# Optimization experiments

Measured on AMD Instinct MI355X. Metric: run time of the kernel, lower is better.

Reference implementation:

```python
import jax, jax.numpy as jnp
import numpy as np

S = 3072      # total tokens across all images
DIM = 1280    # hidden_size
H = 16        # num_heads
HD = DIM // H # head_dim = 80
NSEG = 6      # number of images (cu_seqlens has NSEG+1 entries)


def _rotate_half(x):
    x1, x2 = jnp.split(x, 2, axis=-1)
    return jnp.concatenate([-x2, x1], axis=-1)


def setup_inputs() -> dict:
    key = jax.random.key(0)
    ks = jax.random.split(key, 12)
    hidden_states = jax.random.normal(ks[0], (S, DIM), jnp.float32)
    # realistic vision rotary embedding: half-dim inv_freq, repeated to head_dim
    inv_freq = 1.0 / (10000.0 ** (jnp.arange(0, HD // 2, dtype=jnp.float32) / (HD // 2)))
    freqs = jnp.arange(S, dtype=jnp.float32)[:, None] * inv_freq[None, :]  # [S, HD/2]
    emb = jnp.concatenate([freqs, freqs], axis=-1)  # [S, HD]
    cos = jnp.cos(emb)
    sin = jnp.sin(emb)
    sc = 0.02
    wq = jax.random.normal(ks[1], (DIM, DIM), jnp.float32) * sc
    bq = jax.random.normal(ks[2], (DIM,), jnp.float32) * sc
    wk = jax.random.normal(ks[3], (DIM, DIM), jnp.float32) * sc
    bk = jax.random.normal(ks[4], (DIM,), jnp.float32) * sc
    wv = jax.random.normal(ks[5], (DIM, DIM), jnp.float32) * sc
    bv = jax.random.normal(ks[6], (DIM,), jnp.float32) * sc
    wo = jax.random.normal(ks[7], (DIM, DIM), jnp.float32) * sc
    bo = jax.random.normal(ks[8], (DIM,), jnp.float32) * sc
    cu_seqlens = (jnp.arange(NSEG + 1, dtype=jnp.int32) * (S // NSEG))  # [0,512,...,3072]
    return dict(hidden_states=hidden_states, cos=cos, sin=sin,
                wq=wq, bq=bq, wk=wk, bk=bk, wv=wv, bv=bv, wo=wo, bo=bo,
                cu_seqlens=cu_seqlens)


def reference(hidden_states, cos, sin, wq, bq, wk, bk, wv, bv, wo, bo, cu_seqlens):
    seq_length = hidden_states.shape[0]
    scaling = HD ** (-0.5)
    # QKV projections (torch Linear: x @ W.T + b)
    q = (hidden_states @ wq.T + bq).reshape(seq_length, H, HD)
    k = (hidden_states @ wk.T + bk).reshape(seq_length, H, HD)
    v = (hidden_states @ wv.T + bv).reshape(seq_length, H, HD)
    # apply_rotary_pos_emb_vision: cos/sin [S, HD] broadcast over head axis
    c = cos[:, None, :]
    s = sin[:, None, :]
    q = q * c + _rotate_half(q) * s
    k = k * c + _rotate_half(k) * s
    # block-diagonal (per-image) attention via segment mask
    seg = jnp.searchsorted(cu_seqlens[1:], jnp.arange(seq_length), side='right')
    mask = seg[:, None] == seg[None, :]  # [S, S] bool
    scores = jnp.einsum('shd,thd->hst', q, k) * scaling  # [H, S, S]
    scores = jnp.where(mask[None, :, :], scores, jnp.finfo(scores.dtype).min)
    attn = jax.nn.softmax(scores, axis=-1)
    out = jnp.einsum('hst,thd->shd', attn, v).reshape(seq_length, DIM)
    return out @ wo.T + bo
```

## Files before the change

### kernel.cpp

```cpp
#include <hip/hip_runtime.h>
#include <hip/hip_bf16.h>
#include <hip/hip_fp16.h>
#include <cstdint>
#include <cstddef>

typedef _Float16 f16;
typedef f16 f16x2 __attribute__((ext_vector_type(2)));
typedef f16 f16x4 __attribute__((ext_vector_type(4)));
typedef f16 f16x8 __attribute__((ext_vector_type(8)));
typedef float f32x4 __attribute__((ext_vector_type(4)));

#define S_LEN 3072
#define DIM 1280
#define NH 16
#define HD 80
#define SEG 512

#define MFMA16F(a, b, c) __builtin_amdgcn_mfma_f32_16x16x32_f16((a), (b), (c), 0, 0, 0)

__device__ __forceinline__ void gl2lds16(const void* g, void* l) {
    __builtin_amdgcn_global_load_lds(
        (const __attribute__((address_space(1))) unsigned int*)g,
        (__attribute__((address_space(3))) unsigned int*)l, 16, 0, 0);
}

__device__ __forceinline__ unsigned int pack2(float a, float b) {
    f16x2 t = {(f16)a, (f16)b};
    union { f16x2 v; unsigned int u; } c;
    c.v = t;
    return c.u;
}

__global__ __launch_bounds__(256) void cvt_kernel(
    const float* __restrict__ hs,
    const float* __restrict__ wq, const float* __restrict__ wk,
    const float* __restrict__ wv, const float* __restrict__ wo,
    f16* __restrict__ hs16,
    f16* __restrict__ wq16, f16* __restrict__ wk16,
    f16* __restrict__ wv16, f16* __restrict__ wo16)
{
    const int m = blockIdx.y;
    const float* src; f16* dst; int n4;
    if (m == 0)      { src = hs; dst = hs16; n4 = S_LEN * DIM / 4; }
    else if (m == 1) { src = wq; dst = wq16; n4 = DIM * DIM / 4; }
    else if (m == 2) { src = wk; dst = wk16; n4 = DIM * DIM / 4; }
    else if (m == 3) { src = wv; dst = wv16; n4 = DIM * DIM / 4; }
    else             { src = wo; dst = wo16; n4 = DIM * DIM / 4; }
    int idx = blockIdx.x * 256 + threadIdx.x;
    if (idx >= n4) return;
    f32x4 v = *(const f32x4*)(src + (size_t)idx * 4);
    f16x4 o;
#pragma unroll
    for (int e = 0; e < 4; ++e) o[e] = (f16)v[e];
    *(f16x4*)(dst + (size_t)idx * 4) = o;
}

__global__ __launch_bounds__(512, 2) void gemm_qkv192(
    const f16* __restrict__ A, const f16* __restrict__ Wb,
    const float* __restrict__ bq, const float* __restrict__ bk,
    const float* __restrict__ bv,
    f16* __restrict__ q16, f16* __restrict__ k16, f16* __restrict__ vT)
{
    const int bid = blockIdx.x;
    const int xcd = bid & 7;
    const int idx = bid >> 3;
    const int mt = xcd * 2 + idx / 15;
    const int nt = idx % 15;
    const int m0 = mt * 192;
    const int n0 = nt * 256;

    __shared__ __align__(16) f16 Abuf[2][192 * 64];
    __shared__ __align__(16) f16 Bbuf[2][256 * 64];

    const int tid = threadIdx.x;
    const int w = tid >> 6;
    const int lane = tid & 63;
    const int lane15 = lane & 15;
    const int quad = lane >> 4;
    const int wm = (w >> 2) * 96;
    const int wn = (w & 3) * 64;

    const int srow = lane >> 3;
    const int schk = (lane & 7) ^ srow;

    const int aRow = w * 24;
    const int bRow = (w & 3) * 64 + (w >> 2) * 16;

    const f16* gA = A + (size_t)(m0 + aRow + srow) * DIM + schk * 8;
    const f16* gB = Wb + (size_t)(n0 + bRow + srow) * DIM + schk * 8;

    const int x7 = lane15 & 7;
    const int cc0 = (quad ^ x7) * 8;
    const int cc1 = ((quad + 4) ^ x7) * 8;

    f32x4 acc[6][4];
#pragma unroll
    for (int i = 0; i < 6; ++i)
#pragma unroll
        for (int j = 0; j < 4; ++j)
            acc[i][j] = (f32x4){0.f, 0.f, 0.f, 0.f};

    {
        f16* lA = Abuf[0] + aRow * 64;
        gl2lds16(gA, lA);
        gl2lds16(gA + 8 * DIM, lA + 512);
        gl2lds16(gA + 16 * DIM, lA + 1024);
        f16* lB = Bbuf[0] + bRow * 64;
        gl2lds16(gB, lB);
        gl2lds16(gB + 8 * DIM, lB + 512);
        gl2lds16(gB + 32 * DIM, lB + 2048);
        gl2lds16(gB + 40 * DIM, lB + 2560);
    }

    for (int kt = 0; kt < 20; ++kt) {
        const int s = kt & 1;
        const int sn = s ^ 1;
        const int kn = (kt < 19) ? (kt + 1) : 19;
        const f16* As = Abuf[s];
        const f16* Bsl = Bbuf[s];
        const f16* gAn = gA + kn * 64;
        const f16* gBn = gB + kn * 64;

        asm volatile("s_waitcnt vmcnt(2)" ::: "memory");
        __builtin_amdgcn_s_barrier();
        __builtin_amdgcn_sched_barrier(0);
        {
            f16* lA = Abuf[sn] + aRow * 64;
            gl2lds16(gAn, lA);
            gl2lds16(gAn + 8 * DIM, lA + 512);
            gl2lds16(gAn + 16 * DIM, lA + 1024);
        }
        f16x8 a0[3][2], b01[2][2];
#pragma unroll
        for (int i = 0; i < 3; ++i) {
            const f16* rp = As + (wm + i * 16 + lane15) * 64;
            a0[i][0] = *(const f16x8*)(rp + cc0);
            a0[i][1] = *(const f16x8*)(rp + cc1);
        }
#pragma unroll
        for (int j = 0; j < 2; ++j) {
            const f16* rp = Bsl + (wn + j * 16 + lane15) * 64;
            b01[j][0] = *(const f16x8*)(rp + cc0);
            b01[j][1] = *(const f16x8*)(rp + cc1);
        }
        __builtin_amdgcn_s_setprio(1);
#pragma unroll
        for (int i = 0; i < 3; ++i)
#pragma unroll
            for (int j = 0; j < 2; ++j) {
                acc[i][j] = MFMA16F(a0[i][0], b01[j][0], acc[i][j]);
                acc[i][j] = MFMA16F(a0[i][1], b01[j][1], acc[i][j]);
            }
        __builtin_amdgcn_s_setprio(0);

        asm volatile("s_waitcnt vmcnt(3)" ::: "memory");
        __builtin_amdgcn_s_barrier();
        __builtin_amdgcn_sched_barrier(0);
        {
            f16* lB = Bbuf[sn] + bRow * 64;
            gl2lds16(gBn, lB);
            gl2lds16(gBn + 8 * DIM, lB + 512);
        }
        f16x8 b23[2][2];
#pragma unroll
        for (int j = 0; j < 2; ++j) {
            const f16* rp = Bsl + (wn + 32 + j * 16 + lane15) * 64;
            b23[j][0] = *(const f16x8*)(rp + cc0);
            b23[j][1] = *(const f16x8*)(rp + cc1);
        }
        __builtin_amdgcn_s_setprio(1);
#pragma unroll
        for (int i = 0; i < 3; ++i)
#pragma unroll
            for (int j = 0; j < 2; ++j) {
                acc[i][j + 2] = MFMA16F(a0[i][0], b23[j][0], acc[i][j + 2]);
                acc[i][j + 2] = MFMA16F(a0[i][1], b23[j][1], acc[i][j + 2]);
            }
        __builtin_amdgcn_s_setprio(0);

        __builtin_amdgcn_s_barrier();
        __builtin_amdgcn_sched_barrier(0);
        {
            f16* lB = Bbuf[sn] + bRow * 64 + 2048;
            gl2lds16(gBn + 32 * DIM, lB);
            gl2lds16(gBn + 40 * DIM, lB + 512);
        }
        f16x8 a1[3][2];
#pragma unroll
        for (int i = 0; i < 3; ++i) {
            const f16* rp = As + (wm + 48 + i * 16 + lane15) * 64;
            a1[i][0] = *(const f16x8*)(rp + cc0);
            a1[i][1] = *(const f16x8*)(rp + cc1);
        }
        __builtin_amdgcn_s_setprio(1);
#pragma unroll
        for (int i = 0; i < 3; ++i)
#pragma unroll
            for (int j = 0; j < 2; ++j) {
                acc[i + 3][j + 2] = MFMA16F(a1[i][0], b23[j][0], acc[i + 3][j + 2]);
                acc[i + 3][j + 2] = MFMA16F(a1[i][1], b23[j][1], acc[i + 3][j + 2]);
            }
        __builtin_amdgcn_s_setprio(0);

        __builtin_amdgcn_s_barrier();
        __builtin_amdgcn_sched_barrier(0);
        __builtin_amdgcn_s_setprio(1);
#pragma unroll
        for (int i = 0; i < 3; ++i)
#pragma unroll
            for (int j = 0; j < 2; ++j) {
                acc[i + 3][j] = MFMA16F(a1[i][0], b01[j][0], acc[i + 3][j]);
                acc[i + 3][j] = MFMA16F(a1[i][1], b01[j][1], acc[i + 3][j]);
            }
        __builtin_amdgcn_s_setprio(0);
    }
    asm volatile("s_waitcnt vmcnt(0)" ::: "memory");

    const int sel = nt / 5;
    const int nc0 = (nt % 5) * 256 + wn;
    const float* bias = (sel == 0) ? bq : (sel == 1) ? bk : bv;
    float bvv[4];
#pragma unroll
    for (int j = 0; j < 4; ++j) bvv[j] = bias[nc0 + j * 16 + lane15];

    if (sel < 2) {
        f16* O = sel ? k16 : q16;
#pragma unroll
        for (int i = 0; i < 6; ++i)
#pragma unroll
            for (int j = 0; j < 4; ++j)
#pragma unroll
                for (int r = 0; r < 4; ++r) {
                    int row = m0 + wm + i * 16 + quad * 4 + r;
                    O[(size_t)row * DIM + nc0 + j * 16 + lane15] =
                        (f16)(acc[i][j][r] + bvv[j]);
                }
    } else {
#pragma unroll
        for (int i = 0; i < 6; ++i)
#pragma unroll
            for (int j = 0; j < 4; ++j) {
                f16x4 ov;
#pragma unroll
                for (int r = 0; r < 4; ++r) ov[r] = (f16)(acc[i][j][r] + bvv[j]);
                int row = m0 + wm + i * 16 + quad * 4;
                int col = nc0 + j * 16 + lane15;
                *(f16x4*)(vT + (size_t)col * S_LEN + row) = ov;
            }
    }
}

__global__ __launch_bounds__(256) void gemm_out_kernel(
    const f16* __restrict__ A, const f16* __restrict__ W,
    const float* __restrict__ bias, float* __restrict__ OF)
{
    const int f = blockIdx.x;
    const int xcd = f & 7;
    const int idx = f >> 3;
    const int xt = xcd * 6 + idx % 6;
    const int yt = idx / 6;

    __shared__ __align__(16) f16 As[64 * 32];
    __shared__ __align__(16) f16 Bs[128 * 32];

    const int tid = threadIdx.x;
    const int lane = tid & 63;
    const int lane15 = tid & 15;
    const int quad = lane >> 4;
    const int w = tid >> 6;
    const int wn = w * 32;
    const int m0 = xt * 64;
    const int n0 = yt * 128;

    const int srA = w * 16 + (lane >> 2);
    const int srB = w * 32 + (lane >> 2);
    const int scol = (lane & 3) * 8;
    const f16* gA0 = A + (size_t)(m0 + srA) * DIM + scol;
    const f16* gB0 = W + (size_t)(n0 + srB) * DIM + scol;
    const f16* gB1 = W + (size_t)(n0 + srB + 16) * DIM + scol;
    f16* lA0 = As + (w * 16) * 32;
    f16* lB0 = Bs + (w * 32) * 32;
    f16* lB1 = Bs + (w * 32 + 16) * 32;

    f32x4 acc[4][2];
#pragma unroll
    for (int i = 0; i < 4; ++i)
#pragma unroll
        for (int j = 0; j < 2; ++j)
            acc[i][j] = (f32x4){0.f, 0.f, 0.f, 0.f};

    for (int kt = 0; kt < DIM / 32; ++kt) {
        __syncthreads();
        gl2lds16(gA0 + kt * 32, lA0);
        gl2lds16(gB0 + kt * 32, lB0);
        gl2lds16(gB1 + kt * 32, lB1);
        __syncthreads();

        f16x8 fa[4], fb[2];
#pragma unroll
        for (int i = 0; i < 4; ++i)
            fa[i] = *(const f16x8*)(As + (i * 16 + lane15) * 32 + quad * 8);
#pragma unroll
        for (int j = 0; j < 2; ++j)
            fb[j] = *(const f16x8*)(Bs + (wn + j * 16 + lane15) * 32 + quad * 8);
#pragma unroll
        for (int i = 0; i < 4; ++i)
#pragma unroll
            for (int j = 0; j < 2; ++j)
                acc[i][j] = MFMA16F(fa[i], fb[j], acc[i][j]);
    }

    float bvv[2];
#pragma unroll
    for (int j = 0; j < 2; ++j)
        bvv[j] = bias[n0 + wn + j * 16 + lane15];

#pragma unroll
    for (int i = 0; i < 4; ++i)
#pragma unroll
        for (int j = 0; j < 2; ++j)
#pragma unroll
            for (int r = 0; r < 4; ++r) {
                int row = m0 + i * 16 + quad * 4 + r;
                int col = n0 + wn + j * 16 + lane15;
                OF[(size_t)row * DIM + col] = acc[i][j][r] + bvv[j];
            }
}

__global__ __launch_bounds__(256) void rope_kernel(
    f16* __restrict__ qb, f16* __restrict__ kb,
    const float* __restrict__ cosb, const float* __restrict__ sinb)
{
    int idx = blockIdx.x * 256 + threadIdx.x;
    int c = idx % 5;
    int t = idx / 5;
    int h = t & 15; t >>= 4;
    int s = t % S_LEN;
    int which = t / S_LEN;
    f16* buf = which ? kb : qb;
    float scale = which ? 1.0f : 0.11180339887498948f;
    int j = c * 8;
    f32x4 ca = *(const f32x4*)(cosb + s * HD + j);
    f32x4 cb = *(const f32x4*)(cosb + s * HD + j + 4);
    f32x4 sna = *(const f32x4*)(sinb + s * HD + j);
    f32x4 snb = *(const f32x4*)(sinb + s * HD + j + 4);
    size_t base = (size_t)s * DIM + h * HD + j;
    f16x8 x1 = *(f16x8*)(buf + base);
    f16x8 x2 = *(f16x8*)(buf + base + 40);
    f16x8 o1, o2;
#pragma unroll
    for (int e = 0; e < 8; ++e) {
        float ce = (e < 4) ? ca[e] : cb[e - 4];
        float se = (e < 4) ? sna[e] : snb[e - 4];
        float a = (float)x1[e], b = (float)x2[e];
        o1[e] = (f16)((a * ce - b * se) * scale);
        o2[e] = (f16)((b * ce + a * se) * scale);
    }
    *(f16x8*)(buf + base) = o1;
    *(f16x8*)(buf + base + 40) = o2;
}

__global__ __launch_bounds__(256) void attn_kernel(
    const f16* __restrict__ q, const f16* __restrict__ k,
    const f16* __restrict__ vT, f16* __restrict__ o)
{
    const int h = blockIdx.x;
    const int g = blockIdx.y;
    const int qc = blockIdx.z;
    const int tid = threadIdx.x;
    const int lane15 = tid & 15;
    const int quad = (tid & 63) >> 4;
    const int w = tid >> 6;
    const int qbase = g * SEG + qc * 64;
    const int qrow = qbase + w * 16 + lane15;

    __shared__ __align__(16) f16 Ks[128 * 88];
    __shared__ __align__(16) f16 Vt[80 * 128];

    f16x8 zf;
#pragma unroll
    for (int e = 0; e < 8; ++e) zf[e] = (f16)0.0f;

    f16x8 fq[3];
#pragma unroll
    for (int kc = 0; kc < 3; ++kc) {
        if (kc == 2 && quad >= 2) fq[kc] = zf;
        else fq[kc] = *(const f16x8*)(q + (size_t)qrow * DIM + h * HD + kc * 32 + quad * 8);
    }

    float m_run = -1e30f, l_run = 0.f;
    f32x4 Oa[5];
#pragma unroll
    for (int dt = 0; dt < 5; ++dt) Oa[dt] = (f32x4){0.f, 0.f, 0.f, 0.f};

    for (int kt = 0; kt < 4; ++kt) {
        __syncthreads();
        const int kb = g * SEG + kt * 128;
#pragma unroll
        for (int c = tid; c < 1280; c += 256) {
            int r = c / 10;
            int c8 = (c - r * 10) * 8;
            *(f16x8*)(Ks + r * 88 + c8) =
                *(const f16x8*)(k + (size_t)(kb + r) * DIM + h * HD + c8);
        }
#pragma unroll
        for (int c = tid; c < 1280; c += 256) {
            int d = c >> 4;
            int sc = c & 15;
            *(f16x8*)(Vt + d * 128 + (sc ^ (d & 7)) * 8) =
                *(const f16x8*)(vT + (size_t)(h * HD + d) * S_LEN + kb + sc * 8);
        }
        __syncthreads();

        f32x4 sa[8];
#pragma unroll
        for (int nt = 0; nt < 8; ++nt) sa[nt] = (f32x4){0.f, 0.f, 0.f, 0.f};
#pragma unroll
        for (int kc = 0; kc < 3; ++kc) {
#pragma unroll
            for (int nt = 0; nt < 8; ++nt) {
                f16x8 fk;
                if (kc == 2 && quad >= 2) fk = zf;
                else fk = *(const f16x8*)(Ks + (nt * 16 + lane15) * 88 + kc * 32 + quad * 8);
                sa[nt] = MFMA16F(fk, fq[kc], sa[nt]);
            }
        }

        float mt = -1e30f;
#pragma unroll
        for (int nt = 0; nt < 8; ++nt)
#pragma unroll
            for (int r = 0; r < 4; ++r) mt = fmaxf(mt, sa[nt][r]);
        mt = fmaxf(mt, __shfl_xor(mt, 16, 64));
        mt = fmaxf(mt, __shfl_xor(mt, 32, 64));

        float mn = fmaxf(m_run, mt);
        float alpha = __expf(m_run - mn);
        m_run = mn;
        float lt = 0.f;
        unsigned int pp[8][2];
#pragma unroll
        for (int nt = 0; nt < 8; ++nt) {
            float p0 = __expf(sa[nt][0] - mn);
            float p1 = __expf(sa[nt][1] - mn);
            float p2 = __expf(sa[nt][2] - mn);
            float p3 = __expf(sa[nt][3] - mn);
            lt += (p0 + p1) + (p2 + p3);
            pp[nt][0] = pack2(p0, p1);
            pp[nt][1] = pack2(p2, p3);
        }
        lt += __shfl_xor(lt, 16, 64);
        lt += __shfl_xor(lt, 32, 64);
        l_run = l_run * alpha + lt;

#pragma unroll
        for (int dt = 0; dt < 5; ++dt)
#pragma unroll
            for (int r = 0; r < 4; ++r) Oa[dt][r] *= alpha;

        const int srcA = ((quad & 1) * 2) * 16 + lane15;
        const int srcB = srcA + 16;
        const bool hi = quad >= 2;
#pragma unroll
        for (int kc2 = 0; kc2 < 4; ++kc2) {
            unsigned int e0 = __shfl((int)pp[2 * kc2][0], srcA, 64);
            unsigned int e1 = __shfl((int)pp[2 * kc2][1], srcA, 64);
            unsigned int e2 = __shfl((int)pp[2 * kc2][0], srcB, 64);
            unsigned int e3 = __shfl((int)pp[2 * kc2][1], srcB, 64);
            unsigned int o0 = __shfl((int)pp[2 * kc2 + 1][0], srcA, 64);
            unsigned int o1 = __shfl((int)pp[2 * kc2 + 1][1], srcA, 64);
            unsigned int o2 = __shfl((int)pp[2 * kc2 + 1][0], srcB, 64);
            unsigned int o3 = __shfl((int)pp[2 * kc2 + 1][1], srcB, 64);
            union { unsigned int u[4]; f16x8 v; } fp;
            fp.u[0] = hi ? o0 : e0;
            fp.u[1] = hi ? o1 : e1;
            fp.u[2] = hi ? o2 : e2;
            fp.u[3] = hi ? o3 : e3;
#pragma unroll
            for (int dt = 0; dt < 5; ++dt) {
                int drow = dt * 16 + lane15;
                int slot = (kc2 * 4 + quad) ^ (drow & 7);
                f16x8 fv = *(const f16x8*)(Vt + drow * 128 + slot * 8);
                Oa[dt] = MFMA16F(fv, fp.v, Oa[dt]);
            }
        }
    }

    float inv = 1.0f / l_run;
#pragma unroll
    for (int dt = 0; dt < 5; ++dt) {
        f16x4 ov;
#pragma unroll
        for (int r = 0; r < 4; ++r) ov[r] = (f16)(Oa[dt][r] * inv);
        *(f16x4*)(o + (size_t)qrow * DIM + h * HD + dt * 16 + quad * 4) = ov;
    }
}

extern "C" void kernel_launch(void* const* d_in, const int* in_sizes, int n_in,
                              void* d_out, int out_size, void* d_ws, size_t ws_size,
                              hipStream_t stream)
{
    const float* hs   = (const float*)d_in[0];
    const float* cosb = (const float*)d_in[1];
    const float* sinb = (const float*)d_in[2];
    const float* wq   = (const float*)d_in[3];
    const float* bq   = (const float*)d_in[4];
    const float* wk   = (const float*)d_in[5];
    const float* bk   = (const float*)d_in[6];
    const float* wv   = (const float*)d_in[7];
    const float* bv   = (const float*)d_in[8];
    const float* wo   = (const float*)d_in[9];
    const float* bo   = (const float*)d_in[10];

    const size_t SD = (size_t)S_LEN * DIM;
    const size_t WW = (size_t)DIM * DIM;
    f16* hs16 = (f16*)d_ws;
    f16* wq16 = hs16 + SD;
    f16* wk16 = wq16 + WW;
    f16* wv16 = wk16 + WW;
    f16* wo16 = wv16 + WW;
    f16* q16  = wo16 + WW;
    f16* k16  = q16 + SD;
    f16* vT16 = k16 + SD;
    f16* ao16 = vT16 + SD;
    float* outb = (float*)d_out;

    cvt_kernel<<<dim3(S_LEN * DIM / 4 / 256, 5), 256, 0, stream>>>(
        hs, wq, wk, wv, wo, hs16, wq16, wk16, wv16, wo16);
    gemm_qkv192<<<240, 512, 0, stream>>>(
        hs16, wq16, bq, bk, bv, q16, k16, vT16);
    rope_kernel<<<1920, 256, 0, stream>>>(q16, k16, cosb, sinb);
    attn_kernel<<<dim3(NH, 6, 8), 256, 0, stream>>>(q16, k16, vT16, ao16);
    gemm_out_kernel<<<480, 256, 0, stream>>>(ao16, wo16, bo, outb);
}
```

Baseline: 223.2 us.

## Software-pipeline QKV GEMM main loop by prefetching next k-tile fragments into registers

Restructures the QKV projection GEMM main loop so the A and first-B fragments for the next k-tile are read from LDS during the current iteration's MFMA phases. The prologue now waits for the first tile and preloads fragments, and the per-iteration barriers and vmcnt waits are regrouped. The aim is to hide LDS read latency behind matrix-core work and cut exposed barrier stalls. In exchange it raises register pressure with extra fragment buffers and adds a full vmcnt(0) wait at the end of each iteration, which could serialize global loads.

```diff
diff --git a/kernel.cpp b/kernel.cpp
--- a/kernel.cpp
+++ b/kernel.cpp
@@ -111,57 +111,44 @@
         gl2lds16(gB + 32 * DIM, lB + 2048);
         gl2lds16(gB + 40 * DIM, lB + 2560);
     }
-
+    asm volatile("s_waitcnt vmcnt(0)" ::: "memory");
+    __builtin_amdgcn_s_barrier();
+
+    f16x8 a0[3][2], a1[3][2], b01a[2][2], b01b[2][2], b23[2][2];
+#pragma unroll
+    for (int j = 0; j < 2; ++j) {
+        const f16* rp = Bbuf[0] + (wn + j * 16 + lane15) * 64;
+        b01a[j][0] = *(const f16x8*)(rp + cc0);
+        b01a[j][1] = *(const f16x8*)(rp + cc1);
+    }
+#pragma unroll
+    for (int i = 0; i < 3; ++i) {
+        const f16* rp = Abuf[0] + (wm + i * 16 + lane15) * 64;
+        a0[i][0] = *(const f16x8*)(rp + cc0);
+        a0[i][1] = *(const f16x8*)(rp + cc1);
+    }
+
+#pragma unroll 2
     for (int kt = 0; kt < 20; ++kt) {
         const int s = kt & 1;
         const int sn = s ^ 1;
         const int kn = (kt < 19) ? (kt + 1) : 19;
         const f16* As = Abuf[s];
         const f16* Bsl = Bbuf[s];
+        const f16* Asn = Abuf[sn];
+        const f16* Bsn = Bbuf[sn];
         const f16* gAn = gA + kn * 64;
         const f16* gBn = gB + kn * 64;
 
-        asm volatile("s_waitcnt vmcnt(2)" ::: "memory");
-        __builtin_amdgcn_s_barrier();
-        __builtin_amdgcn_sched_barrier(0);
         {
             f16* lA = Abuf[sn] + aRow * 64;
             gl2lds16(gAn, lA);
             gl2lds16(gAn + 8 * DIM, lA + 512);
             gl2lds16(gAn + 16 * DIM, lA + 1024);
-        }
-        f16x8 a0[3][2], b01[2][2];
-#pragma unroll
-        for (int i = 0; i < 3; ++i) {
-            const f16* rp = As + (wm + i * 16 + lane15) * 64;
-            a0[i][0] = *(const f16x8*)(rp + cc0);
-            a0[i][1] = *(const f16x8*)(rp + cc1);
-        }
-#pragma unroll
-        for (int j = 0; j < 2; ++j) {
-            const f16* rp = Bsl + (wn + j * 16 + lane15) * 64;
-            b01[j][0] = *(const f16x8*)(rp + cc0);
-            b01[j][1] = *(const f16x8*)(rp + cc1);
-        }
-        __builtin_amdgcn_s_setprio(1);
-#pragma unroll
-        for (int i = 0; i < 3; ++i)
-#pragma unroll
-            for (int j = 0; j < 2; ++j) {
-                acc[i][j] = MFMA16F(a0[i][0], b01[j][0], acc[i][j]);
-                acc[i][j] = MFMA16F(a0[i][1], b01[j][1], acc[i][j]);
-            }
-        __builtin_amdgcn_s_setprio(0);
-
-        asm volatile("s_waitcnt vmcnt(3)" ::: "memory");
-        __builtin_amdgcn_s_barrier();
-        __builtin_amdgcn_sched_barrier(0);
-        {
             f16* lB = Bbuf[sn] + bRow * 64;
             gl2lds16(gBn, lB);
             gl2lds16(gBn + 8 * DIM, lB + 512);
         }
-        f16x8 b23[2][2];
 #pragma unroll
         for (int j = 0; j < 2; ++j) {
             const f16* rp = Bsl + (wn + 32 + j * 16 + lane15) * 64;
@@ -173,19 +160,18 @@
         for (int i = 0; i < 3; ++i)
 #pragma unroll
             for (int j = 0; j < 2; ++j) {
-                acc[i][j + 2] = MFMA16F(a0[i][0], b23[j][0], acc[i][j + 2]);
-                acc[i][j + 2] = MFMA16F(a0[i][1], b23[j][1], acc[i][j + 2]);
+                acc[i][j] = MFMA16F(a0[i][0], b01a[j][0], acc[i][j]);
+                acc[i][j] = MFMA16F(a0[i][1], b01a[j][1], acc[i][j]);
             }
         __builtin_amdgcn_s_setprio(0);
-
         __builtin_amdgcn_s_barrier();
         __builtin_amdgcn_sched_barrier(0);
+
         {
             f16* lB = Bbuf[sn] + bRow * 64 + 2048;
             gl2lds16(gBn + 32 * DIM, lB);
             gl2lds16(gBn + 40 * DIM, lB + 512);
         }
-        f16x8 a1[3][2];
 #pragma unroll
         for (int i = 0; i < 3; ++i) {
             const f16* rp = As + (wm + 48 + i * 16 + lane15) * 64;
@@ -197,24 +183,56 @@
         for (int i = 0; i < 3; ++i)
 #pragma unroll
             for (int j = 0; j < 2; ++j) {
+                acc[i][j + 2] = MFMA16F(a0[i][0], b23[j][0], acc[i][j + 2]);
+                acc[i][j + 2] = MFMA16F(a0[i][1], b23[j][1], acc[i][j + 2]);
+            }
+        __builtin_amdgcn_s_setprio(0);
+        __builtin_amdgcn_sched_barrier(0);
+
+        asm volatile("s_waitcnt vmcnt(2)" ::: "memory");
+        __builtin_amdgcn_s_barrier();
+        __builtin_amdgcn_sched_barrier(0);
+#pragma unroll
+        for (int j = 0; j < 2; ++j) {
+            const f16* rp = Bsn + (wn + j * 16 + lane15) * 64;
+            b01b[j][0] = *(const f16x8*)(rp + cc0);
+            b01b[j][1] = *(const f16x8*)(rp + cc1);
+        }
+        __builtin_amdgcn_s_setprio(1);
+#pragma unroll
+        for (int i = 0; i < 3; ++i)
+#pragma unroll
+            for (int j = 0; j < 2; ++j) {
                 acc[i + 3][j + 2] = MFMA16F(a1[i][0], b23[j][0], acc[i + 3][j + 2]);
                 acc[i + 3][j + 2] = MFMA16F(a1[i][1], b23[j][1], acc[i + 3][j + 2]);
             }
         __builtin_amdgcn_s_setprio(0);
-
+        __builtin_amdgcn_sched_barrier(0);
+
+#pragma unroll
+        for (int i = 0; i < 3; ++i) {
+            const f16* rp = Asn + (wm + i * 16 + lane15) * 64;
+            a0[i][0] = *(const f16x8*)(rp + cc0);
+            a0[i][1] = *(const f16x8*)(rp + cc1);
+        }
+        __builtin_amdgcn_s_setprio(1);
+#pragma unroll
+        for (int i = 0; i < 3; ++i)
+#pragma unroll
+            for (int j = 0; j < 2; ++j) {
+                acc[i + 3][j] = MFMA16F(a1[i][0], b01a[j][0], acc[i + 3][j]);
+                acc[i + 3][j] = MFMA16F(a1[i][1], b01a[j][1], acc[i + 3][j]);
+            }
+        __builtin_amdgcn_s_setprio(0);
+#pragma unroll
+        for (int j = 0; j < 2; ++j) {
+            b01a[j][0] = b01b[j][0];
+            b01a[j][1] = b01b[j][1];
+        }
+        asm volatile("s_waitcnt vmcnt(0)" ::: "memory");
         __builtin_amdgcn_s_barrier();
         __builtin_amdgcn_sched_barrier(0);
-        __builtin_amdgcn_s_setprio(1);
-#pragma unroll
-        for (int i = 0; i < 3; ++i)
-#pragma unroll
-            for (int j = 0; j < 2; ++j) {
-                acc[i + 3][j] = MFMA16F(a1[i][0], b01[j][0], acc[i + 3][j]);
-                acc[i + 3][j] = MFMA16F(a1[i][1], b01[j][1], acc[i + 3][j]);
-            }
-        __builtin_amdgcn_s_setprio(0);
-    }
-    asm volatile("s_waitcnt vmcnt(0)" ::: "memory");
+    }
 
     const int sel = nt / 5;
     const int nc0 = (nt % 5) * 256 + wn;
```

Measured after the change: 217.9 us. -2.4%, faster.

## Deepen QKV GEMM pipeline to prefetch two K-tiles ahead with register prefetch

Applied to the files above, without the earlier changes.

Restructures the QKV projection GEMM main loop so global-to-LDS loads are issued two K-steps ahead instead of one. LDS fragment reads for the next MFMA phase are software-pipelined so they overlap the current MFMAs. Barriers are paired with explicit lgkmcnt/vmcnt waits. The goal is to hide global memory latency and LDS read latency behind MFMA work, at the cost of more in-flight loads, more live registers and subtle buffer-reuse ordering risks.

```diff
diff --git a/kernel.cpp b/kernel.cpp
--- a/kernel.cpp
+++ b/kernel.cpp
@@ -101,48 +101,56 @@
             acc[i][j] = (f32x4){0.f, 0.f, 0.f, 0.f};
 
     {
-        f16* lA = Abuf[0] + aRow * 64;
-        gl2lds16(gA, lA);
-        gl2lds16(gA + 8 * DIM, lA + 512);
-        gl2lds16(gA + 16 * DIM, lA + 1024);
         f16* lB = Bbuf[0] + bRow * 64;
         gl2lds16(gB, lB);
         gl2lds16(gB + 8 * DIM, lB + 512);
         gl2lds16(gB + 32 * DIM, lB + 2048);
         gl2lds16(gB + 40 * DIM, lB + 2560);
+        f16* lA = Abuf[0] + aRow * 64;
+        gl2lds16(gA, lA);
+        gl2lds16(gA + 8 * DIM, lA + 512);
+        gl2lds16(gA + 16 * DIM, lA + 1024);
+        f16* lB1 = Bbuf[1] + bRow * 64;
+        gl2lds16(gB + 64, lB1);
+        gl2lds16(gB + 8 * DIM + 64, lB1 + 512);
+        gl2lds16(gB + 32 * DIM + 64, lB1 + 2048);
+        gl2lds16(gB + 40 * DIM + 64, lB1 + 2560);
+        f16* lA1 = Abuf[1] + aRow * 64;
+        gl2lds16(gA + 64, lA1);
+        gl2lds16(gA + 8 * DIM + 64, lA1 + 512);
+        gl2lds16(gA + 16 * DIM + 64, lA1 + 1024);
+    }
+    asm volatile("s_waitcnt vmcnt(7)" ::: "memory");
+    __builtin_amdgcn_s_barrier();
+
+    f16x8 a0[3][2], a1[3][2], b01[2][2], b23[2][2];
+#pragma unroll
+    for (int i = 0; i < 3; ++i) {
+        const f16* rp = Abuf[0] + (wm + i * 16 + lane15) * 64;
+        a0[i][0] = *(const f16x8*)(rp + cc0);
+        a0[i][1] = *(const f16x8*)(rp + cc1);
+    }
+#pragma unroll
+    for (int j = 0; j < 2; ++j) {
+        const f16* rp = Bbuf[0] + (wn + j * 16 + lane15) * 64;
+        b01[j][0] = *(const f16x8*)(rp + cc0);
+        b01[j][1] = *(const f16x8*)(rp + cc1);
     }
 
     for (int kt = 0; kt < 20; ++kt) {
         const int s = kt & 1;
         const int sn = s ^ 1;
-        const int kn = (kt < 19) ? (kt + 1) : 19;
+        const int k2 = (kt + 2 < 20) ? kt + 2 : 19;
         const f16* As = Abuf[s];
         const f16* Bsl = Bbuf[s];
-        const f16* gAn = gA + kn * 64;
-        const f16* gBn = gB + kn * 64;
-
-        asm volatile("s_waitcnt vmcnt(2)" ::: "memory");
+        const f16* Asn = Abuf[sn];
+        const f16* Bsn = Bbuf[sn];
+        const f16* gA2 = gA + k2 * 64;
+        const f16* gB2 = gB + k2 * 64;
+
         __builtin_amdgcn_s_barrier();
-        __builtin_amdgcn_sched_barrier(0);
-        {
-            f16* lA = Abuf[sn] + aRow * 64;
-            gl2lds16(gAn, lA);
-            gl2lds16(gAn + 8 * DIM, lA + 512);
-            gl2lds16(gAn + 16 * DIM, lA + 1024);
-        }
-        f16x8 a0[3][2], b01[2][2];
-#pragma unroll
-        for (int i = 0; i < 3; ++i) {
-            const f16* rp = As + (wm + i * 16 + lane15) * 64;
-            a0[i][0] = *(const f16x8*)(rp + cc0);
-            a0[i][1] = *(const f16x8*)(rp + cc1);
-        }
-#pragma unroll
-        for (int j = 0; j < 2; ++j) {
-            const f16* rp = Bsl + (wn + j * 16 + lane15) * 64;
-            b01[j][0] = *(const f16x8*)(rp + cc0);
-            b01[j][1] = *(const f16x8*)(rp + cc1);
-        }
+        asm volatile("s_waitcnt lgkmcnt(0)" ::: "memory");
+        __builtin_amdgcn_sched_barrier(0);
         __builtin_amdgcn_s_setprio(1);
 #pragma unroll
         for (int i = 0; i < 3; ++i)
@@ -152,22 +160,17 @@
                 acc[i][j] = MFMA16F(a0[i][1], b01[j][1], acc[i][j]);
             }
         __builtin_amdgcn_s_setprio(0);
-
-        asm volatile("s_waitcnt vmcnt(3)" ::: "memory");
-        __builtin_amdgcn_s_barrier();
-        __builtin_amdgcn_sched_barrier(0);
-        {
-            f16* lB = Bbuf[sn] + bRow * 64;
-            gl2lds16(gBn, lB);
-            gl2lds16(gBn + 8 * DIM, lB + 512);
-        }
-        f16x8 b23[2][2];
+        __builtin_amdgcn_sched_barrier(0);
 #pragma unroll
         for (int j = 0; j < 2; ++j) {
             const f16* rp = Bsl + (wn + 32 + j * 16 + lane15) * 64;
             b23[j][0] = *(const f16x8*)(rp + cc0);
             b23[j][1] = *(const f16x8*)(rp + cc1);
         }
+
+        __builtin_amdgcn_s_barrier();
+        asm volatile("s_waitcnt lgkmcnt(0)" ::: "memory");
+        __builtin_amdgcn_sched_barrier(0);
         __builtin_amdgcn_s_setprio(1);
 #pragma unroll
         for (int i = 0; i < 3; ++i)
@@ -177,21 +180,25 @@
                 acc[i][j + 2] = MFMA16F(a0[i][1], b23[j][1], acc[i][j + 2]);
             }
         __builtin_amdgcn_s_setprio(0);
-
-        __builtin_amdgcn_s_barrier();
-        __builtin_amdgcn_sched_barrier(0);
-        {
-            f16* lB = Bbuf[sn] + bRow * 64 + 2048;
-            gl2lds16(gBn + 32 * DIM, lB);
-            gl2lds16(gBn + 40 * DIM, lB + 512);
-        }
-        f16x8 a1[3][2];
+        __builtin_amdgcn_sched_barrier(0);
 #pragma unroll
         for (int i = 0; i < 3; ++i) {
             const f16* rp = As + (wm + 48 + i * 16 + lane15) * 64;
             a1[i][0] = *(const f16x8*)(rp + cc0);
             a1[i][1] = *(const f16x8*)(rp + cc1);
         }
+        {
+            f16* lB = Bbuf[s] + bRow * 64;
+            gl2lds16(gB2, lB);
+            gl2lds16(gB2 + 8 * DIM, lB + 512);
+            gl2lds16(gB2 + 32 * DIM, lB + 2048);
+            gl2lds16(gB2 + 40 * DIM, lB + 2560);
+        }
+        asm volatile("s_waitcnt vmcnt(4)" ::: "memory");
+
+        __builtin_amdgcn_s_barrier();
+        asm volatile("s_waitcnt lgkmcnt(0)" ::: "memory");
+        __builtin_amdgcn_sched_barrier(0);
         __builtin_amdgcn_s_setprio(1);
 #pragma unroll
         for (int i = 0; i < 3; ++i)
@@ -201,8 +208,22 @@
                 acc[i + 3][j + 2] = MFMA16F(a1[i][1], b23[j][1], acc[i + 3][j + 2]);
             }
         __builtin_amdgcn_s_setprio(0);
+        __builtin_amdgcn_sched_barrier(0);
+#pragma unroll
+        for (int i = 0; i < 3; ++i) {
+            const f16* rp = Asn + (wm + i * 16 + lane15) * 64;
+            a0[i][0] = *(const f16x8*)(rp + cc0);
+            a0[i][1] = *(const f16x8*)(rp + cc1);
+        }
+        {
+            f16* lA = Abuf[s] + aRow * 64;
+            gl2lds16(gA2, lA);
+            gl2lds16(gA2 + 8 * DIM, lA + 512);
+            gl2lds16(gA2 + 16 * DIM, lA + 1024);
+        }
 
         __builtin_amdgcn_s_barrier();
+        asm volatile("s_waitcnt lgkmcnt(0)" ::: "memory");
         __builtin_amdgcn_sched_barrier(0);
         __builtin_amdgcn_s_setprio(1);
 #pragma unroll
@@ -213,8 +234,15 @@
                 acc[i + 3][j] = MFMA16F(a1[i][1], b01[j][1], acc[i + 3][j]);
             }
         __builtin_amdgcn_s_setprio(0);
-    }
-    asm volatile("s_waitcnt vmcnt(0)" ::: "memory");
+        __builtin_amdgcn_sched_barrier(0);
+#pragma unroll
+        for (int j = 0; j < 2; ++j) {
+            const f16* rp = Bsn + (wn + j * 16 + lane15) * 64;
+            b01[j][0] = *(const f16x8*)(rp + cc0);
+            b01[j][1] = *(const f16x8*)(rp + cc1);
+        }
+    }
+    asm volatile("s_waitcnt vmcnt(0) lgkmcnt(0)" ::: "memory");
 
     const int sel = nt / 5;
     const int nc0 = (nt % 5) * 256 + wn;
```

Measured after the change: 215.0 us. -3.7%, faster.
